# Kernel optimization log

Measured on AMD Instinct MI355X. Metric: run time of the kernel, lower is better.

## Reference

```python
import jax, jax.numpy as jnp
import numpy as np

B, S, E = 8, 2048, 1024
DROPOUT_P = 0.1


def setup_inputs() -> dict:
    key = jax.random.key(0)
    kq, kk, kv, km, kw, kb = jax.random.split(key, 6)
    query = jax.random.normal(kq, (B, S, E), dtype=jnp.float32)
    key_t = jax.random.normal(kk, (B, S, E), dtype=jnp.float32)
    value = jax.random.normal(kv, (B, S, E), dtype=jnp.float32)
    # inverted dropout mask: keep with prob 1-p, scale kept by 1/(1-p)
    keep = jax.random.bernoulli(km, 1.0 - DROPOUT_P, (B, S, S))
    dropout_mask = keep.astype(jnp.float32) / (1.0 - DROPOUT_P)
    Wout = jax.random.normal(kw, (E, E), dtype=jnp.float32) * (E ** -0.5)
    bout = jax.random.normal(kb, (E,), dtype=jnp.float32) * 0.01
    return {
        "query": query,
        "key": key_t,
        "value": value,
        "dropout_mask": dropout_mask,
        "Wout": Wout,
        "bout": bout,
        "inv_scale_factor": 32,  # sqrt(E) = sqrt(1024)
    }


def reference(query, key, value, dropout_mask, Wout, bout, inv_scale_factor):
    # scores: [B, S, S]
    scores = jnp.einsum("bqd,bkd->bqk", query, key) / jnp.float32(inv_scale_factor)
    probs = jax.nn.softmax(scores, axis=-1)
    probs = probs * dropout_mask  # inverted dropout
    attn = jnp.einsum("bqk,bkd->bqd", probs, value)  # [B, S, E]
    # fc_out: torch Linear -> x @ W.T + b
    return jnp.einsum("bqd,ed->bqe", attn, Wout) + bout
```

## Files before the change

### kernel.cpp

```cpp
#include <hip/hip_runtime.h>
#include <cstdint>
#include <cstddef>

typedef short short8 __attribute__((ext_vector_type(8)));
typedef float f32x4 __attribute__((ext_vector_type(4)));

static __device__ __forceinline__ ushort f2bf(float f) {
  union { float f; uint32_t u; } v; v.f = f;
  uint32_t u = v.u + 0x7fffu + ((v.u >> 16) & 1u);
  return (ushort)(u >> 16);
}
static __device__ __forceinline__ float b2f(uint32_t u) {
  union { uint32_t u; float f; } v; v.u = u << 16;
  return v.f;
}

static __device__ __forceinline__ void g2lds16(const ushort* g, ushort* lds) {
  __builtin_amdgcn_global_load_lds(
      (const __attribute__((address_space(1))) void*)(uintptr_t)g,
      (__attribute__((address_space(3))) void*)(uintptr_t)lds,
      16, 0, 0);
}

#define VMW(n) asm volatile("s_waitcnt vmcnt(" #n ")" ::: "memory")
#define BAR()  asm volatile("s_barrier" ::: "memory")

__global__ __launch_bounds__(256) void convert_qk_bf16(
    const float* __restrict__ Q, const float* __restrict__ K,
    ushort* __restrict__ Qb, ushort* __restrict__ Kb) {
  const bool second = blockIdx.x >= 8192;
  const float* src = second ? K : Q;
  ushort* dst = second ? Kb : Qb;
  const size_t i = ((size_t)(blockIdx.x & 8191) * 256 + threadIdx.x) * 8;
  const float4 a = *(const float4*)(src + i);
  const float4 b = *(const float4*)(src + i + 4);
  ushort4 o0, o1;
  o0.x = f2bf(a.x); o0.y = f2bf(a.y); o0.z = f2bf(a.z); o0.w = f2bf(a.w);
  o1.x = f2bf(b.x); o1.y = f2bf(b.y); o1.z = f2bf(b.z); o1.w = f2bf(b.w);
  *(ushort4*)(dst + i) = o0;
  *(ushort4*)(dst + i + 4) = o1;
}

__global__ __launch_bounds__(256) void convert_w_bf16(
    const float* __restrict__ W, ushort* __restrict__ Wb) {
  const size_t i = ((size_t)blockIdx.x * 256 + threadIdx.x) * 8;
  const float4 a = *(const float4*)(W + i);
  const float4 b = *(const float4*)(W + i + 4);
  ushort4 o0, o1;
  o0.x = f2bf(a.x); o0.y = f2bf(a.y); o0.z = f2bf(a.z); o0.w = f2bf(a.w);
  o1.x = f2bf(b.x); o1.y = f2bf(b.y); o1.z = f2bf(b.z); o1.w = f2bf(b.w);
  *(ushort4*)(Wb + i) = o0;
  *(ushort4*)(Wb + i + 4) = o1;
}

__global__ __launch_bounds__(256) void transpose_convert_v(
    const float* __restrict__ V, ushort* __restrict__ Vt) {
  __shared__ float t[32][33];
  const int b = blockIdx.z;
  const int d0 = blockIdx.x * 32;
  const int k0 = blockIdx.y * 32;
  const int tx = threadIdx.x, ty = threadIdx.y;
  const float* Vb = V + (size_t)b * 2048 * 1024;
  ushort* Vtb = Vt + (size_t)b * 1024 * 2048;
#pragma unroll
  for (int j = 0; j < 32; j += 8)
    t[ty + j][tx] = Vb[(size_t)(k0 + ty + j) * 1024 + d0 + tx];
  __syncthreads();
  const int l = ty * 32 + tx;
  const int kk = (l & 15) * 2;
  const int dd = l >> 4;
#pragma unroll
  for (int p = 0; p < 2; ++p) {
    const int d = dd + p * 16;
    const uint32_t val =
        (uint32_t)f2bf(t[kk][d]) | ((uint32_t)f2bf(t[kk + 1][d]) << 16);
    *(uint32_t*)&Vtb[(size_t)(d0 + d) * 2048 + k0 + kk] = val;
  }
}

template <bool OUT_BF16, bool BIAS>
__global__ __launch_bounds__(512, 2) void gemm256(
    const ushort* __restrict__ Ap, const ushort* __restrict__ Bp,
    void* __restrict__ Cp, int M, int N, int K,
    size_t sA, size_t sB, size_t sC, float scale,
    const float* __restrict__ bias) {
  constexpr int BK = 32;
  __shared__ __align__(16) ushort As[4][256 * BK];
  __shared__ __align__(16) ushort Bs[4][256 * BK];
  const int tid = threadIdx.x;

  const int gx = gridDim.x, gy = gridDim.y;
  const int nwg = gx * gy * gridDim.z;
  int li = blockIdx.x + gx * (blockIdx.y + gy * blockIdx.z);
  li = (li & 7) * (nwg >> 3) + (li >> 3);
  const int bn = li % gx;
  const int rst = li / gx;
  const int bm = rst % gy;
  const int z = rst / gy;

  const int lane = tid & 63, w = tid >> 6;
  const int quad = lane >> 4, l16 = lane & 15;
  const int wm = w >> 2, wn = w & 3;
  const int NT = K >> 5;

  f32x4 acc[8][4];
#pragma unroll
  for (int i = 0; i < 8; ++i)
#pragma unroll
    for (int j = 0; j < 4; ++j) acc[i][j] = (f32x4){0.f, 0.f, 0.f, 0.f};

  const int srow = w * 16 + (lane >> 2);
  const int sgran = (lane & 3) ^ ((lane >> 3) & 3);
  const ushort* Abase = Ap + sA * z + (size_t)bm * 256 * K;
  const ushort* Bbase = Bp + sB * z + (size_t)bn * 256 * K;
  const ushort* Ag0 = Abase + (size_t)srow * K + sgran * 8;
  const ushort* Ag1 = Ag0 + (size_t)128 * K;
  const ushort* Bg0 = Bbase + (size_t)srow * K + sgran * 8;
  const ushort* Bg1 = Bg0 + (size_t)128 * K;
  const int ldsw0 = (w * 16) * BK;
  const int ldsw1 = (128 + w * 16) * BK;

  auto STAGE_A = [&](int t) {
    ushort* a = As[t & 3];
    const size_t ko = (size_t)t * BK;
    g2lds16(Ag0 + ko, a + ldsw0);
    g2lds16(Ag1 + ko, a + ldsw1);
  };
  auto STAGE_B = [&](int t) {
    ushort* b = Bs[t & 3];
    const size_t ko = (size_t)t * BK;
    g2lds16(Bg0 + ko, b + ldsw0);
    g2lds16(Bg1 + ko, b + ldsw1);
  };

  const int pg = quad ^ ((l16 >> 1) & 3);
  const int aoff = (wm * 128 + l16) * BK + pg * 8;
  const int boff = (wn * 64 + l16) * BK + pg * 8;

  auto TILE = [&](int t, bool stage_ok) {
    const ushort* a = As[t & 3];
    const ushort* b = Bs[t & 3];
    short8 bfv[4], af[4];
#pragma unroll
    for (int tn = 0; tn < 4; ++tn)
      bfv[tn] = *(const short8*)&b[boff + tn * 16 * BK];
#pragma unroll
    for (int tm = 0; tm < 4; ++tm)
      af[tm] = *(const short8*)&a[aoff + tm * 16 * BK];
    if (stage_ok) STAGE_A(t + 3);
    BAR();
    __builtin_amdgcn_s_setprio(1);
#pragma unroll
    for (int tm = 0; tm < 4; ++tm)
#pragma unroll
      for (int tn = 0; tn < 4; ++tn)
        acc[tm][tn] = __builtin_amdgcn_mfma_f32_16x16x32_bf16(
            af[tm], bfv[tn], acc[tm][tn], 0, 0, 0);
    __builtin_amdgcn_s_setprio(0);
    BAR();
    short8 af2[4];
#pragma unroll
    for (int tm = 0; tm < 4; ++tm)
      af2[tm] = *(const short8*)&a[aoff + (4 + tm) * 16 * BK];
    if (stage_ok) STAGE_B(t + 3);
    BAR();
    __builtin_amdgcn_s_setprio(1);
#pragma unroll
    for (int tm = 0; tm < 4; ++tm)
#pragma unroll
      for (int tn = 0; tn < 4; ++tn)
        acc[4 + tm][tn] = __builtin_amdgcn_mfma_f32_16x16x32_bf16(
            af2[tm], bfv[tn], acc[4 + tm][tn], 0, 0, 0);
    __builtin_amdgcn_s_setprio(0);
  };

  STAGE_A(0); STAGE_B(0);
  STAGE_A(1); STAGE_B(1);
  STAGE_A(2); STAGE_B(2);
  for (int t = 0; t < NT - 2; ++t) {
    VMW(8);
    BAR();
    TILE(t, t + 3 < NT);
  }
  VMW(4);
  BAR();
  TILE(NT - 2, false);
  VMW(0);
  BAR();
  TILE(NT - 1, false);

  const size_t cz = sC * z;
#pragma unroll
  for (int tn = 0; tn < 4; ++tn) {
    const int gc = bn * 256 + wn * 64 + tn * 16 + l16;
    const float bv = BIAS ? bias[gc] : 0.f;
#pragma unroll
    for (int tm = 0; tm < 8; ++tm) {
      const int grb = bm * 256 + wm * 128 + tm * 16 + quad * 4;
#pragma unroll
      for (int r = 0; r < 4; ++r) {
        const float v = acc[tm][tn][r] * scale + bv;
        const size_t idx = (size_t)(grb + r) * N + gc;
        if constexpr (OUT_BF16)
          ((ushort*)Cp + cz)[idx] = f2bf(v);
        else
          ((float*)Cp + cz)[idx] = v;
      }
    }
  }
}

__global__ __launch_bounds__(256) void softmax_dropout(
    ushort* __restrict__ P, const float* __restrict__ mask) {
  const int row = blockIdx.x;
  const size_t off = (size_t)row * 2048 + (size_t)threadIdx.x * 8;
  ushort* p = P + off;
  const float* mk = mask + off;
  const uint4 raw = *(const uint4*)p;
  float s[8];
  s[0] = b2f(raw.x & 0xffffu); s[1] = b2f(raw.x >> 16);
  s[2] = b2f(raw.y & 0xffffu); s[3] = b2f(raw.y >> 16);
  s[4] = b2f(raw.z & 0xffffu); s[5] = b2f(raw.z >> 16);
  s[6] = b2f(raw.w & 0xffffu); s[7] = b2f(raw.w >> 16);
  float m = s[0];
#pragma unroll
  for (int i = 1; i < 8; ++i) m = fmaxf(m, s[i]);
#pragma unroll
  for (int o = 32; o >= 1; o >>= 1) m = fmaxf(m, __shfl_xor(m, o));
  __shared__ float redm[4], reds[4];
  const int wv = threadIdx.x >> 6;
  if ((threadIdx.x & 63) == 0) redm[wv] = m;
  __syncthreads();
  m = fmaxf(fmaxf(redm[0], redm[1]), fmaxf(redm[2], redm[3]));
  float e[8], l = 0.f;
#pragma unroll
  for (int i = 0; i < 8; ++i) { e[i] = __expf(s[i] - m); l += e[i]; }
#pragma unroll
  for (int o = 32; o >= 1; o >>= 1) l += __shfl_xor(l, o);
  if ((threadIdx.x & 63) == 0) reds[wv] = l;
  __syncthreads();
  l = (reds[0] + reds[1]) + (reds[2] + reds[3]);
  const float inv = 1.0f / l;
  const float4 m0 = *(const float4*)mk;
  const float4 m1 = *(const float4*)(mk + 4);
  float q[8];
  q[0] = e[0] * inv * m0.x; q[1] = e[1] * inv * m0.y;
  q[2] = e[2] * inv * m0.z; q[3] = e[3] * inv * m0.w;
  q[4] = e[4] * inv * m1.x; q[5] = e[5] * inv * m1.y;
  q[6] = e[6] * inv * m1.z; q[7] = e[7] * inv * m1.w;
  uint4 o;
  o.x = (uint32_t)f2bf(q[0]) | ((uint32_t)f2bf(q[1]) << 16);
  o.y = (uint32_t)f2bf(q[2]) | ((uint32_t)f2bf(q[3]) << 16);
  o.z = (uint32_t)f2bf(q[4]) | ((uint32_t)f2bf(q[5]) << 16);
  o.w = (uint32_t)f2bf(q[6]) | ((uint32_t)f2bf(q[7]) << 16);
  *(uint4*)p = o;
}

extern "C" void kernel_launch(void* const* d_in, const int* in_sizes, int n_in,
                              void* d_out, int out_size, void* d_ws,
                              size_t ws_size, hipStream_t stream) {
  (void)in_sizes; (void)n_in; (void)out_size; (void)ws_size;
  const float* Q    = (const float*)d_in[0];
  const float* Kmat = (const float*)d_in[1];
  const float* V    = (const float*)d_in[2];
  const float* mask = (const float*)d_in[3];
  const float* W    = (const float*)d_in[4];
  const float* bout = (const float*)d_in[5];
  float* out = (float*)d_out;

  ushort* RegA = (ushort*)d_ws;
  ushort* RegB = RegA + (size_t)16 * 1024 * 1024;
  ushort* P    = RegB + (size_t)16 * 1024 * 1024;

  convert_qk_bf16<<<dim3(16384), 256, 0, stream>>>(Q, Kmat, RegA, RegB);
  gemm256<true, false><<<dim3(8, 8, 8), 512, 0, stream>>>(
      RegA, RegB, P, 2048, 2048, 1024,
      (size_t)2048 * 1024, (size_t)2048 * 1024, (size_t)2048 * 2048,
      1.0f / 32.0f, nullptr);
  transpose_convert_v<<<dim3(32, 64, 8), dim3(32, 8), 0, stream>>>(V, RegA);
  softmax_dropout<<<dim3(16384), 256, 0, stream>>>(P, mask);
  gemm256<true, false><<<dim3(4, 8, 8), 512, 0, stream>>>(
      P, RegA, RegB, 2048, 1024, 2048,
      (size_t)2048 * 2048, (size_t)1024 * 2048, (size_t)2048 * 1024,
      1.0f, nullptr);
  convert_w_bf16<<<dim3(512), 256, 0, stream>>>(W, RegA);
  gemm256<false, true><<<dim3(4, 64, 1), 512, 0, stream>>>(
      RegB, RegA, out, 16384, 1024, 1024, 0, 0, 0, 1.0f, bout);
}
```

Baseline: 542.0 us.

## Fuse softmax and dropout into QK GEMM epilogue with deferred normalization

Removes the standalone softmax_dropout kernel. The QK^T GEMM epilogue now computes exp(score) without subtracting a max, multiplies by the dropout mask, writes bf16, and atomically accumulates row sums into a scratch buffer (the output tensor, zeroed by memset). The PV GEMM epilogue divides by the row sum. This saves a full read/write pass over the S×S probability matrix, but drops max-subtraction and so relies on scores staying small enough not to overflow exp. It also enlarges the V transpose tiles to 64x64.

```diff
diff --git a/kernel.cpp b/kernel.cpp
--- a/kernel.cpp
+++ b/kernel.cpp
@@ -9,10 +9,6 @@
   union { float f; uint32_t u; } v; v.f = f;
   uint32_t u = v.u + 0x7fffu + ((v.u >> 16) & 1u);
   return (ushort)(u >> 16);
-}
-static __device__ __forceinline__ float b2f(uint32_t u) {
-  union { uint32_t u; float f; } v; v.u = u << 16;
-  return v.f;
 }
 
 static __device__ __forceinline__ void g2lds16(const ushort* g, ushort* lds) {
@@ -55,35 +51,35 @@
 
 __global__ __launch_bounds__(256) void transpose_convert_v(
     const float* __restrict__ V, ushort* __restrict__ Vt) {
-  __shared__ float t[32][33];
+  __shared__ float t[64][65];
   const int b = blockIdx.z;
-  const int d0 = blockIdx.x * 32;
-  const int k0 = blockIdx.y * 32;
-  const int tx = threadIdx.x, ty = threadIdx.y;
+  const int d0 = blockIdx.x * 64;
+  const int k0 = blockIdx.y * 64;
   const float* Vb = V + (size_t)b * 2048 * 1024;
   ushort* Vtb = Vt + (size_t)b * 1024 * 2048;
-#pragma unroll
-  for (int j = 0; j < 32; j += 8)
+  const int tx = threadIdx.x & 63, ty = threadIdx.x >> 6;
+#pragma unroll
+  for (int j = 0; j < 64; j += 4)
     t[ty + j][tx] = Vb[(size_t)(k0 + ty + j) * 1024 + d0 + tx];
   __syncthreads();
-  const int l = ty * 32 + tx;
-  const int kk = (l & 15) * 2;
-  const int dd = l >> 4;
-#pragma unroll
-  for (int p = 0; p < 2; ++p) {
-    const int d = dd + p * 16;
+  const int lk = (threadIdx.x & 31) * 2;
+  const int ld = threadIdx.x >> 5;
+#pragma unroll
+  for (int p = 0; p < 8; ++p) {
+    const int d = ld + p * 8;
     const uint32_t val =
-        (uint32_t)f2bf(t[kk][d]) | ((uint32_t)f2bf(t[kk + 1][d]) << 16);
-    *(uint32_t*)&Vtb[(size_t)(d0 + d) * 2048 + k0 + kk] = val;
+        (uint32_t)f2bf(t[lk][d]) | ((uint32_t)f2bf(t[lk + 1][d]) << 16);
+    *(uint32_t*)&Vtb[(size_t)(d0 + d) * 2048 + k0 + lk] = val;
   }
 }
 
-template <bool OUT_BF16, bool BIAS>
+template <int EPI>
 __global__ __launch_bounds__(512, 2) void gemm256(
     const ushort* __restrict__ Ap, const ushort* __restrict__ Bp,
     void* __restrict__ Cp, int M, int N, int K,
     size_t sA, size_t sB, size_t sC, float scale,
-    const float* __restrict__ bias) {
+    const float* __restrict__ bias, const float* __restrict__ mask,
+    float* __restrict__ rowsum) {
   constexpr int BK = 32;
   __shared__ __align__(16) ushort As[4][256 * BK];
   __shared__ __align__(16) ushort Bs[4][256 * BK];
@@ -190,70 +186,75 @@
   TILE(NT - 1, false);
 
   const size_t cz = sC * z;
-#pragma unroll
-  for (int tn = 0; tn < 4; ++tn) {
-    const int gc = bn * 256 + wn * 64 + tn * 16 + l16;
-    const float bv = BIAS ? bias[gc] : 0.f;
+  if constexpr (EPI == 1) {
+    ushort* Cb = (ushort*)Cp + cz;
+    const float* Mb = mask + (size_t)z * 2048 * 2048;
+    float rs[8][4];
+#pragma unroll
+    for (int tm = 0; tm < 8; ++tm)
+#pragma unroll
+      for (int r = 0; r < 4; ++r) rs[tm][r] = 0.f;
 #pragma unroll
     for (int tm = 0; tm < 8; ++tm) {
       const int grb = bm * 256 + wm * 128 + tm * 16 + quad * 4;
 #pragma unroll
       for (int r = 0; r < 4; ++r) {
-        const float v = acc[tm][tn][r] * scale + bv;
-        const size_t idx = (size_t)(grb + r) * N + gc;
-        if constexpr (OUT_BF16)
-          ((ushort*)Cp + cz)[idx] = f2bf(v);
-        else
-          ((float*)Cp + cz)[idx] = v;
+        const size_t rowoff = (size_t)(grb + r) * N;
+        const float* mrow = Mb + rowoff;
+        ushort* crow = Cb + rowoff;
+#pragma unroll
+        for (int tn = 0; tn < 4; ++tn) {
+          const int gc = bn * 256 + wn * 64 + tn * 16 + l16;
+          const float e = __expf(acc[tm][tn][r] * scale);
+          rs[tm][r] += e;
+          crow[gc] = f2bf(e * mrow[gc]);
+        }
+      }
+    }
+#pragma unroll
+    for (int tm = 0; tm < 8; ++tm)
+#pragma unroll
+      for (int r = 0; r < 4; ++r) {
+        float v = rs[tm][r];
+        v += __shfl_xor(v, 1);
+        v += __shfl_xor(v, 2);
+        v += __shfl_xor(v, 4);
+        v += __shfl_xor(v, 8);
+        if (l16 == ((tm * 4 + r) & 15))
+          atomicAdd(&rowsum[(size_t)z * 2048 + bm * 256 + wm * 128 + tm * 16 +
+                            quad * 4 + r],
+                    v);
+      }
+  } else if constexpr (EPI == 2) {
+    ushort* Cb = (ushort*)Cp + cz;
+#pragma unroll
+    for (int tm = 0; tm < 8; ++tm) {
+      const int grb = bm * 256 + wm * 128 + tm * 16 + quad * 4;
+#pragma unroll
+      for (int r = 0; r < 4; ++r) {
+        const float linv = 1.0f / rowsum[(size_t)z * 2048 + grb + r];
+#pragma unroll
+        for (int tn = 0; tn < 4; ++tn) {
+          const int gc = bn * 256 + wn * 64 + tn * 16 + l16;
+          Cb[(size_t)(grb + r) * N + gc] = f2bf(acc[tm][tn][r] * linv);
+        }
+      }
+    }
+  } else {
+    float* Cb = (float*)Cp + cz;
+#pragma unroll
+    for (int tn = 0; tn < 4; ++tn) {
+      const int gc = bn * 256 + wn * 64 + tn * 16 + l16;
+      const float bv = bias[gc];
+#pragma unroll
+      for (int tm = 0; tm < 8; ++tm) {
+        const int grb = bm * 256 + wm * 128 + tm * 16 + quad * 4;
+#pragma unroll
+        for (int r = 0; r < 4; ++r)
+          Cb[(size_t)(grb + r) * N + gc] = acc[tm][tn][r] * scale + bv;
       }
     }
   }
-}
-
-__global__ __launch_bounds__(256) void softmax_dropout(
-    ushort* __restrict__ P, const float* __restrict__ mask) {
-  const int row = blockIdx.x;
-  const size_t off = (size_t)row * 2048 + (size_t)threadIdx.x * 8;
-  ushort* p = P + off;
-  const float* mk = mask + off;
-  const uint4 raw = *(const uint4*)p;
-  float s[8];
-  s[0] = b2f(raw.x & 0xffffu); s[1] = b2f(raw.x >> 16);
-  s[2] = b2f(raw.y & 0xffffu); s[3] = b2f(raw.y >> 16);
-  s[4] = b2f(raw.z & 0xffffu); s[5] = b2f(raw.z >> 16);
-  s[6] = b2f(raw.w & 0xffffu); s[7] = b2f(raw.w >> 16);
-  float m = s[0];
-#pragma unroll
-  for (int i = 1; i < 8; ++i) m = fmaxf(m, s[i]);
-#pragma unroll
-  for (int o = 32; o >= 1; o >>= 1) m = fmaxf(m, __shfl_xor(m, o));
-  __shared__ float redm[4], reds[4];
-  const int wv = threadIdx.x >> 6;
-  if ((threadIdx.x & 63) == 0) redm[wv] = m;
-  __syncthreads();
-  m = fmaxf(fmaxf(redm[0], redm[1]), fmaxf(redm[2], redm[3]));
-  float e[8], l = 0.f;
-#pragma unroll
-  for (int i = 0; i < 8; ++i) { e[i] = __expf(s[i] - m); l += e[i]; }
-#pragma unroll
-  for (int o = 32; o >= 1; o >>= 1) l += __shfl_xor(l, o);
-  if ((threadIdx.x & 63) == 0) reds[wv] = l;
-  __syncthreads();
-  l = (reds[0] + reds[1]) + (reds[2] + reds[3]);
-  const float inv = 1.0f / l;
-  const float4 m0 = *(const float4*)mk;
-  const float4 m1 = *(const float4*)(mk + 4);
-  float q[8];
-  q[0] = e[0] * inv * m0.x; q[1] = e[1] * inv * m0.y;
-  q[2] = e[2] * inv * m0.z; q[3] = e[3] * inv * m0.w;
-  q[4] = e[4] * inv * m1.x; q[5] = e[5] * inv * m1.y;
-  q[6] = e[6] * inv * m1.z; q[7] = e[7] * inv * m1.w;
-  uint4 o;
-  o.x = (uint32_t)f2bf(q[0]) | ((uint32_t)f2bf(q[1]) << 16);
-  o.y = (uint32_t)f2bf(q[2]) | ((uint32_t)f2bf(q[3]) << 16);
-  o.z = (uint32_t)f2bf(q[4]) | ((uint32_t)f2bf(q[5]) << 16);
-  o.w = (uint32_t)f2bf(q[6]) | ((uint32_t)f2bf(q[7]) << 16);
-  *(uint4*)p = o;
 }
 
 extern "C" void kernel_launch(void* const* d_in, const int* in_sizes, int n_in,
@@ -271,19 +272,21 @@
   ushort* RegA = (ushort*)d_ws;
   ushort* RegB = RegA + (size_t)16 * 1024 * 1024;
   ushort* P    = RegB + (size_t)16 * 1024 * 1024;
-
+  float* rowsum = out;
+
+  hipMemsetAsync(rowsum, 0, (size_t)8 * 2048 * sizeof(float), stream);
   convert_qk_bf16<<<dim3(16384), 256, 0, stream>>>(Q, Kmat, RegA, RegB);
-  gemm256<true, false><<<dim3(8, 8, 8), 512, 0, stream>>>(
+  gemm256<1><<<dim3(8, 8, 8), 512, 0, stream>>>(
       RegA, RegB, P, 2048, 2048, 1024,
       (size_t)2048 * 1024, (size_t)2048 * 1024, (size_t)2048 * 2048,
-      1.0f / 32.0f, nullptr);
-  transpose_convert_v<<<dim3(32, 64, 8), dim3(32, 8), 0, stream>>>(V, RegA);
-  softmax_dropout<<<dim3(16384), 256, 0, stream>>>(P, mask);
-  gemm256<true, false><<<dim3(4, 8, 8), 512, 0, stream>>>(
+      1.0f / 32.0f, nullptr, mask, rowsum);
+  transpose_convert_v<<<dim3(16, 32, 8), 256, 0, stream>>>(V, RegA);
+  gemm256<2><<<dim3(4, 8, 8), 512, 0, stream>>>(
       P, RegA, RegB, 2048, 1024, 2048,
       (size_t)2048 * 2048, (size_t)1024 * 2048, (size_t)2048 * 1024,
-      1.0f, nullptr);
+      1.0f, nullptr, nullptr, rowsum);
   convert_w_bf16<<<dim3(512), 256, 0, stream>>>(W, RegA);
-  gemm256<false, true><<<dim3(4, 64, 1), 512, 0, stream>>>(
-      RegB, RegA, out, 16384, 1024, 1024, 0, 0, 0, 1.0f, bout);
-}
+  gemm256<0><<<dim3(4, 64, 1), 512, 0, stream>>>(
+      RegB, RegA, out, 16384, 1024, 1024, 0, 0, 0, 1.0f, bout, nullptr,
+      nullptr);
+}
```

Result: no change. 532.9 us (-1.7%).
